# Kernel optimization log

Hardware: AMD Instinct MI355X
Metric: run time of the kernel (lower is better)

The kernel has to match this reference:

```python
import jax, jax.numpy as jnp
import numpy as np

B, S, D, H = 2, 2048, 768, 12
N = D // H  # head dim = 64
NEG = -1e12


def setup_inputs() -> dict:
    key = jax.random.key(0)
    ks = jax.random.split(key, 6)
    scale = 1.0 / np.sqrt(D)
    return {
        "inputs": jax.random.normal(ks[0], (B, S, D), dtype=jnp.float32),
        "masks": jnp.ones((B, S), dtype=jnp.int32),
        "Wq": jax.random.normal(ks[1], (D, D), dtype=jnp.float32) * scale,
        "bq": jnp.zeros((D,), dtype=jnp.float32),
        "Wk": jax.random.normal(ks[2], (D, D), dtype=jnp.float32) * scale,
        "bk": jnp.zeros((D,), dtype=jnp.float32),
        "Wv": jax.random.normal(ks[3], (D, D), dtype=jnp.float32) * scale,
        "bv": jnp.zeros((D,), dtype=jnp.float32),
        "Wo": jax.random.normal(ks[4], (D, D), dtype=jnp.float32) * scale,
        "bo": jnp.zeros((D,), dtype=jnp.float32),
    }


def reference(inputs, masks, Wq, bq, Wk, bk, Wv, bv, Wo, bo):
    # projections: [B,S,D] -> [B,H,S,N]
    def proj(x, W, b):
        y = jnp.einsum('bsd,df->bsf', x, W) + b
        return y.reshape(B, -1, H, N).transpose(0, 2, 1, 3)

    q = proj(inputs, Wq, bq)
    k = proj(inputs, Wk, bk)
    v = proj(inputs, Wv, bv)

    # scores [B,H,S,S]
    a = jnp.einsum('bhqn,bhkn->bhqk', q, k) / jnp.float32(np.sqrt(N))
    m = masks[:, None, None, :]  # [B,1,1,S]
    a = jnp.where(m == 0, jnp.float32(NEG), a)
    a = jax.nn.softmax(a, axis=-1)

    o = jnp.einsum('bhqk,bhkn->bhqn', a, v)  # [B,H,S,N]
    o = o.transpose(0, 2, 1, 3).reshape(B, -1, H * N)
    return jnp.einsum('bsd,df->bsf', o, Wo) + bo
```

## Files before the change

### kernel.cpp

```cpp
#include <hip/hip_runtime.h>
#include <hip/hip_bf16.h>

#define B_ 2
#define S_ 2048
#define D_ 768
#define H_ 12
#define BS_ (B_*S_)
#define NEGL2 -1.44e12f
#define SCALE2 0.18033688f

typedef __bf16 bf16;
typedef __attribute__((ext_vector_type(8))) __bf16 bf16x8;
typedef __attribute__((ext_vector_type(4))) float f32x4;
typedef __attribute__((ext_vector_type(16))) float f32x16;

__global__ __launch_bounds__(256) void cast_f32_bf16(const float* __restrict__ in,
                                                     bf16* __restrict__ out, int n) {
    int i = (blockIdx.x * 256 + threadIdx.x) * 8;
    if (i + 8 <= n) {
        float4 a = *(const float4*)(in + i);
        float4 b = *(const float4*)(in + i + 4);
        bf16x8 v;
        v[0] = (bf16)a.x; v[1] = (bf16)a.y; v[2] = (bf16)a.z; v[3] = (bf16)a.w;
        v[4] = (bf16)b.x; v[5] = (bf16)b.y; v[6] = (bf16)b.z; v[7] = (bf16)b.w;
        *(bf16x8*)(out + i) = v;
    }
}

__global__ __launch_bounds__(256) void transpose_w4(const float* __restrict__ W0,
                                                    const float* __restrict__ W1,
                                                    const float* __restrict__ W2,
                                                    const float* __restrict__ W3,
                                                    bf16* __restrict__ Wt0) {
    const float* Ws[4] = {W0, W1, W2, W3};
    const float* W = Ws[blockIdx.z];
    bf16* Wt = Wt0 + (size_t)blockIdx.z * D_ * D_;
    __shared__ float tile[16][17];
    int bx = blockIdx.x, by = blockIdx.y;
    int tx = threadIdx.x & 15, ty = threadIdx.x >> 4;
    tile[ty][tx] = W[(by * 16 + ty) * D_ + bx * 16 + tx];
    __syncthreads();
    Wt[(bx * 16 + ty) * D_ + by * 16 + tx] = (bf16)tile[tx][ty];
}

__device__ inline unsigned pk2(float a, float b) {
    union { unsigned u; __bf16 h[2]; } x;
    x.h[0] = (__bf16)a; x.h[1] = (__bf16)b;
    return x.u;
}

__device__ __forceinline__ void gload16(const void* g, void* l) {
    __builtin_amdgcn_global_load_lds(
        (const __attribute__((address_space(1))) unsigned int*)g,
        (__attribute__((address_space(3))) unsigned int*)l, 16, 0, 0);
}

__global__ __launch_bounds__(256) void gemm_qkv(const bf16* __restrict__ A,
                                                const bf16* __restrict__ Bt,
                                                const float* __restrict__ bq,
                                                const float* __restrict__ bk,
                                                const float* __restrict__ bv,
                                                bf16* __restrict__ Qo,
                                                bf16* __restrict__ Ko,
                                                bf16* __restrict__ Vo) {
    constexpr int K = 768;
    __shared__ __align__(16) bf16 As[64 * 64];
    __shared__ __align__(16) bf16 Bs[128 * 64];
    const int bm = blockIdx.x, bn = blockIdx.y;
    const int t = threadIdx.x;
    const int lane = t & 63, wid = t >> 6;
    const int wm = wid >> 1, wn = wid & 1;
    f32x4 acc[2][4] = {};

    const char* gA = (const char*)(A + (size_t)(bm * 64) * K);
    const char* gB = (const char*)(Bt + (size_t)(bn * 128) * K);
    const int srow = wid * 8 + (lane >> 3);
    const int chg = ((lane & 7) ^ (lane >> 3)) * 16;

    for (int kt = 0; kt < 12; ++kt) {
        __syncthreads();
#pragma unroll
        for (int c = 0; c < 2; ++c)
            gload16(gA + (size_t)(c * 32 + srow) * (K * 2) + kt * 128 + chg,
                    (char*)As + c * 4096 + wid * 1024);
#pragma unroll
        for (int c = 0; c < 4; ++c)
            gload16(gB + (size_t)(c * 32 + srow) * (K * 2) + kt * 128 + chg,
                    (char*)Bs + c * 4096 + wid * 1024);
        asm volatile("s_waitcnt vmcnt(0)");
        __syncthreads();

#pragma unroll
        for (int kb = 0; kb < 2; ++kb) {
            const int chunk = ((kb * 4 + (lane >> 4)) ^ (lane & 7)) * 16;
            bf16x8 aF[2], bF[4];
#pragma unroll
            for (int mf = 0; mf < 2; ++mf)
                aF[mf] = *(const bf16x8*)((const char*)As + (wm * 32 + mf * 16 + (lane & 15)) * 128 + chunk);
#pragma unroll
            for (int nf = 0; nf < 4; ++nf)
                bF[nf] = *(const bf16x8*)((const char*)Bs + (wn * 64 + nf * 16 + (lane & 15)) * 128 + chunk);
#pragma unroll
            for (int mf = 0; mf < 2; ++mf)
#pragma unroll
                for (int nf = 0; nf < 4; ++nf)
                    acc[mf][nf] = __builtin_amdgcn_mfma_f32_16x16x32_bf16(aF[mf], bF[nf], acc[mf][nf], 0, 0, 0);
        }
    }

    const int mid = bn / 6;
    const float* bias = (mid == 0) ? bq : (mid == 1) ? bk : bv;
#pragma unroll
    for (int mf = 0; mf < 2; ++mf) {
#pragma unroll
        for (int nf = 0; nf < 4; ++nf) {
#pragma unroll
            for (int r = 0; r < 4; ++r) {
                int row = bm * 64 + wm * 32 + mf * 16 + (lane >> 4) * 4 + r;
                int lc = (bn - mid * 6) * 128 + wn * 64 + nf * 16 + (lane & 15);
                float v = acc[mf][nf][r] + bias[lc];
                if (mid == 0) {
                    Qo[(size_t)row * D_ + lc] = (bf16)(v * SCALE2);
                } else if (mid == 1) {
                    Ko[(size_t)row * D_ + lc] = (bf16)v;
                } else {
                    int bb = row >> 11, s = row & 2047, hh = lc >> 6, nn = lc & 63;
                    Vo[(size_t)(((bb * H_ + hh) << 6) + nn) * S_ + s] = (bf16)v;
                }
            }
        }
    }
}

__global__ __launch_bounds__(256) void gemm_out(const bf16* __restrict__ A,
                                                const bf16* __restrict__ Bt,
                                                const float* __restrict__ bias,
                                                float* __restrict__ Cout) {
    constexpr int K = 768;
    __shared__ __align__(16) bf16 As[32 * 64];
    __shared__ __align__(16) bf16 Bs[128 * 64];
    const int bm = blockIdx.x, bn = blockIdx.y;
    const int t = threadIdx.x;
    const int lane = t & 63, wid = t >> 6;
    const int wm = wid >> 1, wn = wid & 1;
    f32x4 acc[4] = {};

    const char* gA = (const char*)(A + (size_t)(bm * 32) * K);
    const char* gB = (const char*)(Bt + (size_t)(bn * 128) * K);
    const int srow = wid * 8 + (lane >> 3);
    const int chg = ((lane & 7) ^ (lane >> 3)) * 16;

    for (int kt = 0; kt < 12; ++kt) {
        __syncthreads();
        gload16(gA + (size_t)srow * (K * 2) + kt * 128 + chg,
                (char*)As + wid * 1024);
#pragma unroll
        for (int c = 0; c < 4; ++c)
            gload16(gB + (size_t)(c * 32 + srow) * (K * 2) + kt * 128 + chg,
                    (char*)Bs + c * 4096 + wid * 1024);
        asm volatile("s_waitcnt vmcnt(0)");
        __syncthreads();

#pragma unroll
        for (int kb = 0; kb < 2; ++kb) {
            const int chunk = ((kb * 4 + (lane >> 4)) ^ (lane & 7)) * 16;
            bf16x8 aF = *(const bf16x8*)((const char*)As + (wm * 16 + (lane & 15)) * 128 + chunk);
            bf16x8 bF[4];
#pragma unroll
            for (int nf = 0; nf < 4; ++nf)
                bF[nf] = *(const bf16x8*)((const char*)Bs + (wn * 64 + nf * 16 + (lane & 15)) * 128 + chunk);
#pragma unroll
            for (int nf = 0; nf < 4; ++nf)
                acc[nf] = __builtin_amdgcn_mfma_f32_16x16x32_bf16(aF, bF[nf], acc[nf], 0, 0, 0);
        }
    }

#pragma unroll
    for (int nf = 0; nf < 4; ++nf)
#pragma unroll
        for (int r = 0; r < 4; ++r) {
            int row = bm * 32 + wm * 16 + (lane >> 4) * 4 + r;
            int col = bn * 128 + wn * 64 + nf * 16 + (lane & 15);
            Cout[(size_t)row * D_ + col] = acc[nf][r] + bias[col];
        }
}

__global__ __launch_bounds__(512, 2) void attn_fwd6(const bf16* __restrict__ Qs,
                                                    const bf16* __restrict__ Kg,
                                                    const bf16* __restrict__ Vt,
                                                    const int* __restrict__ masks,
                                                    bf16* __restrict__ Oa) {
    __shared__ __align__(16) char Sb[2][2][16384];
    __shared__ float Lr[4][64];

    const int qt = blockIdx.x, bh = blockIdx.y;
    const int b = bh / H_, h = bh % H_;
    const int t = threadIdx.x;
    const int lane = t & 63, w = t >> 6;
    const int lo = lane & 31, hi = lane >> 5;
    const int qs = w & 3, half = w >> 2;

    unsigned long long mflags;
    {
        const int* mb = masks + b * S_ + half * 1024 + lane * 16;
        int anyz = 0;
#pragma unroll
        for (int u = 0; u < 4; ++u) {
            int4 mv = *(const int4*)(mb + u * 4);
            anyz |= (!mv.x) | (!mv.y) | (!mv.z) | (!mv.w);
        }
        mflags = __ballot(anyz != 0);
    }

    bf16x8 bQ[4];
    {
        const bf16* qp = Qs + (size_t)(b * S_ + qt * 128 + qs * 32 + lo) * D_ + h * 64 + 8 * hi;
#pragma unroll
        for (int kb = 0; kb < 4; ++kb) bQ[kb] = *(const bf16x8*)(qp + 16 * kb);
    }

    const int srow = lane >> 3;
    const int swz = ((lane & 7) * 16) ^ ((srow & 7) << 4);
    const int sh = w >> 1, sv = w & 1;
    const char* gsrc;
    size_t cstride, tstep;
    if (sv == 0) {
        gsrc = (const char*)Kg + ((size_t)(b * S_ + sh * 1024 + srow) * D_ + h * 64) * 2 + swz;
        cstride = (size_t)8 * D_ * 2;
        tstep = (size_t)64 * D_ * 2;
    } else {
        gsrc = (const char*)Vt + ((size_t)(bh * 64 + srow) * S_ + sh * 1024) * 2 + swz;
        cstride = (size_t)8 * S_ * 2;
        tstep = 128;
    }
    char* dst0 = &Sb[0][sh][0] + sv * 8192;
    char* dst1 = &Sb[1][sh][0] + sv * 8192;

    auto STAGE = [&](int bi, int kt) {
        const char* p = gsrc + (size_t)kt * tstep;
        char* d = bi ? dst1 : dst0;
#pragma unroll
        for (int j = 0; j < 8; ++j)
            gload16(p + j * cstride, d + j * 1024);
    };

    if (w < 4) STAGE(0, 0);
    asm volatile("s_waitcnt vmcnt(0)");
    __syncthreads();

    f32x16 oo[2] = {};
    float lrun = 0.f;

#pragma unroll 1
    for (int kt = 0; kt < 16; ++kt) {
        const int cur = kt & 1;
        if (w < 4 && kt < 15) STAGE(cur ^ 1, kt + 1);
        const char* Kh = &Sb[cur][half][0];
        const char* Vh = Kh + 8192;
        const bool mk = (mflags >> (4 * kt)) & 0xFULL;
        float lsum = 0.f;
#pragma unroll
        for (int kb2 = 0; kb2 < 2; ++kb2) {
            const int row = kb2 * 32 + lo;
            const int rsw = (row & 7) << 4;
            f32x16 sa = {};
            __builtin_amdgcn_s_setprio(1);
#pragma unroll
            for (int kb = 0; kb < 4; ++kb) {
                bf16x8 aK = *(const bf16x8*)(Kh + row * 128 + ((kb * 32 + hi * 16) ^ rsw));
                sa = __builtin_amdgcn_mfma_f32_32x32x16_bf16(aK, bQ[kb], sa, 0, 0, 0);
            }
            __builtin_amdgcn_s_setprio(0);
            float pp[16];
            if (!mk) {
#pragma unroll
                for (int r = 0; r < 16; ++r) pp[r] = __builtin_amdgcn_exp2f(sa[r]);
            } else {
#pragma unroll
                for (int r = 0; r < 16; ++r) {
                    int kv = half * 1024 + kt * 64 + kb2 * 32 + (r & 3) + 8 * (r >> 2) + 4 * hi;
                    float madd = masks[b * S_ + kv] ? 0.f : NEGL2;
                    pp[r] = __builtin_amdgcn_exp2f(sa[r] + madd);
                }
            }
            float s8[8];
#pragma unroll
            for (int i = 0; i < 8; ++i) s8[i] = pp[i] + pp[i + 8];
            lsum += ((s8[0] + s8[1]) + (s8[2] + s8[3])) + ((s8[4] + s8[5]) + (s8[6] + s8[7]));

#pragma unroll
            for (int ks2 = 0; ks2 < 2; ++ks2) {
                const float* q8 = pp + ks2 * 8;
                unsigned u0 = pk2(q8[0], q8[1]);
                unsigned u1 = pk2(q8[2], q8[3]);
                unsigned u2 = pk2(q8[4], q8[5]);
                unsigned u3 = pk2(q8[6], q8[7]);
                asm("v_permlane32_swap_b32 %0, %1" : "+v"(u0), "+v"(u2));
                asm("v_permlane32_swap_b32 %0, %1" : "+v"(u1), "+v"(u3));
                union { unsigned u[4]; bf16x8 v; } pa;
                pa.u[0] = u0; pa.u[1] = u1; pa.u[2] = u2; pa.u[3] = u3;
                const int ks = kb2 * 2 + ks2;
                __builtin_amdgcn_s_setprio(1);
#pragma unroll
                for (int nb = 0; nb < 2; ++nb) {
                    const int vr = nb * 32 + lo;
                    bf16x8 aV = *(const bf16x8*)(Vh + vr * 128 +
                                                 ((ks * 32 + hi * 16) ^ ((vr & 7) << 4)));
                    oo[nb] = __builtin_amdgcn_mfma_f32_32x32x16_bf16(aV, pa.v, oo[nb], 0, 0, 0);
                }
                __builtin_amdgcn_s_setprio(0);
            }
        }
        lrun += lsum + __shfl_xor(lsum, 32, 64);
        asm volatile("s_waitcnt vmcnt(0)");
        __syncthreads();
    }

    __syncthreads();
    float* Mb = (float*)&Sb[0][0][0];
    if (half == 1) {
        float* d = Mb + qs * 2048;
#pragma unroll
        for (int nb = 0; nb < 2; ++nb)
#pragma unroll
            for (int r = 0; r < 16; ++r) d[(nb * 16 + r) * 64 + lane] = oo[nb][r];
        Lr[qs][lane] = lrun;
    }
    __syncthreads();
    if (half == 0) {
        const float* s = Mb + qs * 2048;
#pragma unroll
        for (int nb = 0; nb < 2; ++nb)
#pragma unroll
            for (int r = 0; r < 16; ++r) oo[nb][r] += s[(nb * 16 + r) * 64 + lane];
        float inv = 1.f / (lrun + Lr[qs][lane]);

        char* ot = (char*)&Sb[0][0][0] + 32768 + qs * 8192;
#pragma unroll
        for (int nb = 0; nb < 2; ++nb)
#pragma unroll
            for (int tq = 0; tq < 4; ++tq) {
                int n0 = tq * 8 + hi * 4 + nb * 32;
                *(unsigned*)(ot + lo * 144 + n0 * 2) =
                    pk2(oo[nb][tq * 4 + 0] * inv, oo[nb][tq * 4 + 1] * inv);
                *(unsigned*)(ot + lo * 144 + n0 * 2 + 4) =
                    pk2(oo[nb][tq * 4 + 2] * inv, oo[nb][tq * 4 + 3] * inv);
            }
#pragma unroll
        for (int pass = 0; pass < 4; ++pass) {
            int chunk = hi + pass * 2;
            bf16x8 vv = *(const bf16x8*)(ot + lo * 144 + chunk * 16);
            *(bf16x8*)(Oa + (size_t)(b * S_ + qt * 128 + qs * 32 + lo) * D_ + h * 64 + chunk * 8) = vv;
        }
    }
}

extern "C" void kernel_launch(void* const* d_in, const int* in_sizes, int n_in,
                              void* d_out, int out_size, void* d_ws, size_t ws_size,
                              hipStream_t stream) {
    (void)in_sizes; (void)n_in; (void)out_size; (void)ws_size;
    const float* x  = (const float*)d_in[0];
    const int* masks = (const int*)d_in[1];
    const float* Wq = (const float*)d_in[2];
    const float* bq = (const float*)d_in[3];
    const float* Wk = (const float*)d_in[4];
    const float* bk = (const float*)d_in[5];
    const float* Wv = (const float*)d_in[6];
    const float* bv = (const float*)d_in[7];
    const float* Wo = (const float*)d_in[8];
    const float* bo = (const float*)d_in[9];
    float* out = (float*)d_out;

    char* ws = (char*)d_ws;
    size_t off = 0;
    auto alloc = [&](size_t bytes) {
        void* p = ws + off;
        off += (bytes + 255) & ~(size_t)255;
        return p;
    };
    bf16* Xb  = (bf16*)alloc((size_t)BS_ * D_ * 2);
    bf16* Wqt = (bf16*)alloc((size_t)D_ * D_ * 2);
    bf16* Wkt = (bf16*)alloc((size_t)D_ * D_ * 2);
    bf16* Wvt = (bf16*)alloc((size_t)D_ * D_ * 2);
    bf16* Wot = (bf16*)alloc((size_t)D_ * D_ * 2);
    bf16* Qb  = (bf16*)alloc((size_t)BS_ * D_ * 2);
    bf16* Kb2 = (bf16*)alloc((size_t)BS_ * D_ * 2);
    bf16* Vtb = (bf16*)alloc((size_t)BS_ * D_ * 2);
    bf16* Ab  = (bf16*)alloc((size_t)BS_ * D_ * 2);
    (void)Wkt; (void)Wvt;

    cast_f32_bf16<<<(BS_ * D_) / 2048, 256, 0, stream>>>(x, Xb, BS_ * D_);
    transpose_w4<<<dim3(48, 48, 4), 256, 0, stream>>>(Wq, Wk, Wv, Wo, Wqt);

    gemm_qkv<<<dim3(64, 18), 256, 0, stream>>>(Xb, Wqt, bq, bk, bv, Qb, Kb2, Vtb);

    attn_fwd6<<<dim3(16, 24), 512, 0, stream>>>(Qb, Kb2, Vtb, masks, Ab);

    gemm_out<<<dim3(128, 6), 256, 0, stream>>>(Ab, Wot, bo, out);
}
```

Measured before the change: 106.6 us.

## Remap attention blocks per XCD and relax the K/V staging waits

The attention grid becomes 1D and each block index is remapped so that all query tiles of a given batch-head land on the same XCD. The goal is for those blocks to share K/V traffic in that XCD's L2. The per-tile sync changes from a full vmcnt(0) wait plus __syncthreads to a split scheme. Loader waves issue the next stage, wait only for the previous stage with vmcnt(8), and raw s_barrier calls with sched_barrier fences mark the top and bottom of each iteration. This lets global loads stay in flight across the barrier, at the cost of an extra barrier per iteration and tighter reliance on getting the counter arithmetic right.

```diff
diff --git a/kernel.cpp b/kernel.cpp
--- a/kernel.cpp
+++ b/kernel.cpp
@@ -185,7 +185,7 @@
         }
 }
 
-__global__ __launch_bounds__(512, 2) void attn_fwd6(const bf16* __restrict__ Qs,
+__global__ __launch_bounds__(512, 2) void attn_fwd9(const bf16* __restrict__ Qs,
                                                     const bf16* __restrict__ Kg,
                                                     const bf16* __restrict__ Vt,
                                                     const int* __restrict__ masks,
@@ -193,7 +193,10 @@
     __shared__ __align__(16) char Sb[2][2][16384];
     __shared__ float Lr[4][64];
 
-    const int qt = blockIdx.x, bh = blockIdx.y;
+    const int id = blockIdx.x;
+    const int xcd = id & 7, j = id >> 3;
+    const int bh = xcd * 3 + (j % 3);
+    const int qt = j / 3;
     const int b = bh / H_, h = bh % H_;
     const int t = threadIdx.x;
     const int lane = t & 63, w = t >> 6;
@@ -240,13 +243,15 @@
         const char* p = gsrc + (size_t)kt * tstep;
         char* d = bi ? dst1 : dst0;
 #pragma unroll
-        for (int j = 0; j < 8; ++j)
-            gload16(p + j * cstride, d + j * 1024);
+        for (int j2 = 0; j2 < 8; ++j2)
+            gload16(p + j2 * cstride, d + j2 * 1024);
     };
 
-    if (w < 4) STAGE(0, 0);
-    asm volatile("s_waitcnt vmcnt(0)");
-    __syncthreads();
+    if (w < 4) {
+        STAGE(0, 0);
+        asm volatile("s_waitcnt vmcnt(0)" ::: "memory");
+    }
+    __builtin_amdgcn_s_barrier();
 
     f32x16 oo[2] = {};
     float lrun = 0.f;
@@ -254,7 +259,17 @@
 #pragma unroll 1
     for (int kt = 0; kt < 16; ++kt) {
         const int cur = kt & 1;
-        if (w < 4 && kt < 15) STAGE(cur ^ 1, kt + 1);
+        if (w < 4) {
+            if (kt < 15) {
+                STAGE(cur ^ 1, kt + 1);
+                asm volatile("s_waitcnt vmcnt(8)" ::: "memory");
+            } else {
+                asm volatile("s_waitcnt vmcnt(0)" ::: "memory");
+            }
+        }
+        __builtin_amdgcn_s_barrier();
+        __builtin_amdgcn_sched_barrier(0);
+
         const char* Kh = &Sb[cur][half][0];
         const char* Vh = Kh + 8192;
         const bool mk = (mflags >> (4 * kt)) & 0xFULL;
@@ -312,8 +327,10 @@
             }
         }
         lrun += lsum + __shfl_xor(lsum, 32, 64);
-        asm volatile("s_waitcnt vmcnt(0)");
-        __syncthreads();
+
+        __builtin_amdgcn_sched_barrier(0);
+        asm volatile("s_waitcnt lgkmcnt(0)" ::: "memory");
+        __builtin_amdgcn_s_barrier();
     }
 
     __syncthreads();
@@ -394,7 +411,7 @@
 
     gemm_qkv<<<dim3(64, 18), 256, 0, stream>>>(Xb, Wqt, bq, bk, bv, Qb, Kb2, Vtb);
 
-    attn_fwd6<<<dim3(16, 24), 512, 0, stream>>>(Qb, Kb2, Vtb, masks, Ab);
+    attn_fwd9<<<dim3(384), 512, 0, stream>>>(Qb, Kb2, Vtb, masks, Ab);
 
     gemm_out<<<dim3(128, 6), 256, 0, stream>>>(Ab, Wot, bo, out);
 }
```

After: 109.5 us. 1.03x slower.

## Shrink attention blocks to 64 queries and stage K/V via registers

Applied to the files above, without the earlier changes.

The attention kernel now uses 256-thread blocks covering 64 query rows instead of 512-thread blocks covering 128, which doubles the grid to 768 blocks. The launch bound asks for three blocks per CU. The double-buffered async global-to-LDS copy is replaced by a single LDS buffer: every wave prefetches the next K/V tile into registers, then writes it to shared memory between two barriers. The aim is better occupancy and load balance across CUs, paid for with an extra barrier per tile, more register pressure from the staging registers, and K/V traffic that is redundant across twice as many blocks.

```diff
diff --git a/kernel.cpp b/kernel.cpp
--- a/kernel.cpp
+++ b/kernel.cpp
@@ -185,20 +185,22 @@
         }
 }
 
-__global__ __launch_bounds__(512, 2) void attn_fwd6(const bf16* __restrict__ Qs,
-                                                    const bf16* __restrict__ Kg,
-                                                    const bf16* __restrict__ Vt,
-                                                    const int* __restrict__ masks,
-                                                    bf16* __restrict__ Oa) {
-    __shared__ __align__(16) char Sb[2][2][16384];
-    __shared__ float Lr[4][64];
+__global__ __launch_bounds__(256, 3) void attn_fwd10(const bf16* __restrict__ Qs,
+                                                     const bf16* __restrict__ Kg,
+                                                     const bf16* __restrict__ Vt,
+                                                     const int* __restrict__ masks,
+                                                     bf16* __restrict__ Oa) {
+    __shared__ __align__(16) char Sbuf[2][16384];
+    __shared__ float Lr[2][64];
 
     const int qt = blockIdx.x, bh = blockIdx.y;
     const int b = bh / H_, h = bh % H_;
     const int t = threadIdx.x;
     const int lane = t & 63, w = t >> 6;
     const int lo = lane & 31, hi = lane >> 5;
-    const int qs = w & 3, half = w >> 2;
+    const int half = w >> 1;
+    const int qs = w & 1;
+    const int role = w & 1;
 
     unsigned long long mflags;
     {
@@ -214,49 +216,47 @@
 
     bf16x8 bQ[4];
     {
-        const bf16* qp = Qs + (size_t)(b * S_ + qt * 128 + qs * 32 + lo) * D_ + h * 64 + 8 * hi;
+        const bf16* qp = Qs + (size_t)(b * S_ + qt * 64 + qs * 32 + lo) * D_ + h * 64 + 8 * hi;
 #pragma unroll
         for (int kb = 0; kb < 4; ++kb) bQ[kb] = *(const bf16x8*)(qp + 16 * kb);
     }
 
     const int srow = lane >> 3;
-    const int swz = ((lane & 7) * 16) ^ ((srow & 7) << 4);
-    const int sh = w >> 1, sv = w & 1;
+    const int scolS = ((lane & 7) * 16) ^ ((srow & 7) << 4);
     const char* gsrc;
     size_t cstride, tstep;
-    if (sv == 0) {
-        gsrc = (const char*)Kg + ((size_t)(b * S_ + sh * 1024 + srow) * D_ + h * 64) * 2 + swz;
+    if (role == 0) {
+        gsrc = (const char*)Kg + ((size_t)(b * S_ + half * 1024 + srow) * D_ + h * 64) * 2 + scolS;
         cstride = (size_t)8 * D_ * 2;
         tstep = (size_t)64 * D_ * 2;
     } else {
-        gsrc = (const char*)Vt + ((size_t)(bh * 64 + srow) * S_ + sh * 1024) * 2 + swz;
+        gsrc = (const char*)Vt + ((size_t)(bh * 64 + srow) * S_ + half * 1024) * 2 + scolS;
         cstride = (size_t)8 * S_ * 2;
         tstep = 128;
     }
-    char* dst0 = &Sb[0][sh][0] + sv * 8192;
-    char* dst1 = &Sb[1][sh][0] + sv * 8192;
-
-    auto STAGE = [&](int bi, int kt) {
-        const char* p = gsrc + (size_t)kt * tstep;
-        char* d = bi ? dst1 : dst0;
-#pragma unroll
-        for (int j = 0; j < 8; ++j)
-            gload16(p + j * cstride, d + j * 1024);
-    };
-
-    if (w < 4) STAGE(0, 0);
-    asm volatile("s_waitcnt vmcnt(0)");
-    __syncthreads();
+    char* dst = &Sbuf[half][0] + role * 8192 + lane * 16;
+    const char* Kh = &Sbuf[half][0];
+    const char* Vh = Kh + 8192;
+
+    bf16x8 sreg[8];
+#pragma unroll
+    for (int j = 0; j < 8; ++j) sreg[j] = *(const bf16x8*)(gsrc + j * cstride);
 
     f32x16 oo[2] = {};
     float lrun = 0.f;
 
 #pragma unroll 1
     for (int kt = 0; kt < 16; ++kt) {
-        const int cur = kt & 1;
-        if (w < 4 && kt < 15) STAGE(cur ^ 1, kt + 1);
-        const char* Kh = &Sb[cur][half][0];
-        const char* Vh = Kh + 8192;
+        __syncthreads();
+#pragma unroll
+        for (int j = 0; j < 8; ++j) *(bf16x8*)(dst + j * 1024) = sreg[j];
+        __syncthreads();
+        if (kt < 15) {
+            const char* p = gsrc + (size_t)(kt + 1) * tstep;
+#pragma unroll
+            for (int j = 0; j < 8; ++j) sreg[j] = *(const bf16x8*)(p + j * cstride);
+        }
+
         const bool mk = (mflags >> (4 * kt)) & 0xFULL;
         float lsum = 0.f;
 #pragma unroll
@@ -312,30 +312,30 @@
             }
         }
         lrun += lsum + __shfl_xor(lsum, 32, 64);
-        asm volatile("s_waitcnt vmcnt(0)");
-        __syncthreads();
     }
 
     __syncthreads();
-    float* Mb = (float*)&Sb[0][0][0];
-    if (half == 1) {
-        float* d = Mb + qs * 2048;
+    float* mbuf = (float*)&Sbuf[0][0];
+    if (w >= 2) {
+        float* d = mbuf + qs * 2048;
 #pragma unroll
         for (int nb = 0; nb < 2; ++nb)
 #pragma unroll
-            for (int r = 0; r < 16; ++r) d[(nb * 16 + r) * 64 + lane] = oo[nb][r];
+            for (int r = 0; r < 16; ++r)
+                d[(nb * 16 + r) * 64 + lane] = oo[nb][r];
         Lr[qs][lane] = lrun;
     }
     __syncthreads();
-    if (half == 0) {
-        const float* s = Mb + qs * 2048;
+    if (w < 2) {
+        const float* s = mbuf + qs * 2048;
 #pragma unroll
         for (int nb = 0; nb < 2; ++nb)
 #pragma unroll
-            for (int r = 0; r < 16; ++r) oo[nb][r] += s[(nb * 16 + r) * 64 + lane];
+            for (int r = 0; r < 16; ++r)
+                oo[nb][r] += s[(nb * 16 + r) * 64 + lane];
         float inv = 1.f / (lrun + Lr[qs][lane]);
 
-        char* ot = (char*)&Sb[0][0][0] + 32768 + qs * 8192;
+        char* ot = (char*)&Sbuf[1][0] + qs * 8192;
 #pragma unroll
         for (int nb = 0; nb < 2; ++nb)
 #pragma unroll
@@ -350,7 +350,7 @@
         for (int pass = 0; pass < 4; ++pass) {
             int chunk = hi + pass * 2;
             bf16x8 vv = *(const bf16x8*)(ot + lo * 144 + chunk * 16);
-            *(bf16x8*)(Oa + (size_t)(b * S_ + qt * 128 + qs * 32 + lo) * D_ + h * 64 + chunk * 8) = vv;
+            *(bf16x8*)(Oa + (size_t)(b * S_ + qt * 64 + qs * 32 + lo) * D_ + h * 64 + chunk * 8) = vv;
         }
     }
 }
@@ -394,7 +394,7 @@
 
     gemm_qkv<<<dim3(64, 18), 256, 0, stream>>>(Xb, Wqt, bq, bk, bv, Qb, Kb2, Vtb);
 
-    attn_fwd6<<<dim3(16, 24), 512, 0, stream>>>(Qb, Kb2, Vtb, masks, Ab);
+    attn_fwd10<<<dim3(32, 24), 256, 0, stream>>>(Qb, Kb2, Vtb, masks, Ab);
 
     gemm_out<<<dim3(128, 6), 256, 0, stream>>>(Ab, Wot, bo, out);
 }
```

Measured after the change: 99.78 us. 6.4% less time.
